# Kernel optimization log

Measured on AMD Instinct MI355X. Metric: run time of the kernel, lower is better.

## Reference

```python
import jax, jax.numpy as jnp
import numpy as np

FRAC_BITS = 16            # fixed-point fractional bits (MPC fixedpoint precision)
SCALE = float(1 << FRAC_BITS)

def fxp(v):
    """Emulate dup_with_precision: round value to the fixed-point grid with
    FRAC_BITS fractional bits. Straight-through (identity) gradient, matching
    the MPC backward pass which propagates gradients through truncation."""
    return v + jax.lax.stop_gradient(jnp.round(v * SCALE) / SCALE - v)


def setup_inputs() -> dict:
    key = jax.random.key(0)
    kx, kw = jax.random.split(key)
    in_dim, out_dim, batch = 4096, 4096, 2048
    x = jax.random.normal(kx, (batch, in_dim), dtype=jnp.float32)
    # Dense_Local init: w ~ N(0, 1/sqrt(in_dim+1)), b = zeros
    w = jax.random.normal(kw, (in_dim, out_dim), dtype=jnp.float32) / np.sqrt(in_dim + 1)
    b = jnp.zeros((out_dim,), dtype=jnp.float32)
    return {"x": x, "w": w, "b": b}


def reference(x, w, b):
    # quantize operands to the fixed-point grid (values live on the grid in MPC)
    xq = fxp(x)
    wq = fxp(w)
    # y = x @ w, then dup_with_precision(x.fixedpoint): truncate product back
    y = fxp(jnp.matmul(xq, wq))           # [batch, out_dim]
    # + bias
    y = y + fxp(b)
    # secure ReLU: s = drelu_local(y) (sign bit), y = relu(y, s) = y * s
    s = y >= 0
    y = jnp.where(s, y, jnp.zeros((), dtype=y.dtype))
    # final dup_with_precision(new_fixedpoint=x.fixedpoint)
    return fxp(y)
```

## Files before the change

### kernel.cpp

```cpp
#include <hip/hip_runtime.h>
#include <hip/hip_bf16.h>
#include <stdint.h>

#define M_DIM 2048
#define N_DIM 4096
#define K_DIM 4096

#define NT 64

typedef short short8 __attribute__((ext_vector_type(8)));
typedef float f32x4 __attribute__((ext_vector_type(4)));

typedef __attribute__((address_space(1))) unsigned int gu32;
typedef __attribute__((address_space(3))) unsigned int lu32;

__device__ static inline unsigned short f32_to_bf16(float f) {
  union { float f; unsigned int u; } v; v.f = f;
  unsigned int u = v.u;
  u += 0x7FFFu + ((u >> 16) & 1u);
  return (unsigned short)(u >> 16);
}

__global__ void cvt_x_kernel(const float* __restrict__ in, unsigned short* __restrict__ out) {
  size_t i = ((size_t)blockIdx.x * blockDim.x + threadIdx.x) * 8;
  f32x4 a = *(const f32x4*)(in + i);
  f32x4 b = *(const f32x4*)(in + i + 4);
  short8 o;
  o[0] = (short)f32_to_bf16(a[0]); o[1] = (short)f32_to_bf16(a[1]);
  o[2] = (short)f32_to_bf16(a[2]); o[3] = (short)f32_to_bf16(a[3]);
  o[4] = (short)f32_to_bf16(b[0]); o[5] = (short)f32_to_bf16(b[1]);
  o[6] = (short)f32_to_bf16(b[2]); o[7] = (short)f32_to_bf16(b[3]);
  *(short8*)(out + i) = o;
}

__global__ void transpose_cvt_w_kernel(const float* __restrict__ w, unsigned short* __restrict__ wt) {
  __shared__ unsigned short tile[64][64 + 8];
  int bn = blockIdx.x * 64;
  int bk = blockIdx.y * 64;
  int t = threadIdx.x;
  int c4 = (t & 15) * 4;
  int r0 = t >> 4;
#pragma unroll
  for (int p = 0; p < 4; ++p) {
    int r = r0 + p * 16;
    f32x4 v = *(const f32x4*)(w + (size_t)(bk + r) * N_DIM + bn + c4);
    tile[c4 + 0][r] = f32_to_bf16(v[0]);
    tile[c4 + 1][r] = f32_to_bf16(v[1]);
    tile[c4 + 2][r] = f32_to_bf16(v[2]);
    tile[c4 + 3][r] = f32_to_bf16(v[3]);
  }
  __syncthreads();
  int orow = t >> 2;
  int oc = (t & 3) * 16;
  short8 lo, hi;
#pragma unroll
  for (int j = 0; j < 8; ++j) {
    lo[j] = (short)tile[orow][oc + j];
    hi[j] = (short)tile[orow][oc + 8 + j];
  }
  unsigned short* op = wt + (size_t)(bn + orow) * K_DIM + bk + oc;
  *(short8*)(op) = lo;
  *(short8*)(op + 8) = hi;
}


__global__ __launch_bounds__(512) void gemm8_kernel(
    const unsigned short* __restrict__ A, const unsigned short* __restrict__ Bt,
    const float* __restrict__ bias, float* __restrict__ C) {
  __shared__ unsigned short smA[3 * 24576];
  char* smemc = (char*)&smA[0];

  const int tid = threadIdx.x;
  const int lane = tid & 63;
  const int w = tid >> 6;
  const int wm = w >> 2, wn = w & 3;

  const int id = blockIdx.x;
  const int x = id & 7, j = id >> 3;
  const int by = ((x >> 2) << 3) + (j >> 2);
  const int bx = ((x & 3) << 2) + (j & 3);
  const int r0 = by * 128, c0 = bx * 256;

  const int l8 = lane >> 3, l7 = lane & 7;
  const int chunkE = ((l7 ^ l8) << 3);
  const unsigned short* Ag = A + (size_t)(r0 + w * 16 + l8) * K_DIM + chunkE;
  const unsigned short* Bg = Bt + (size_t)(c0 + w * 32 + l8) * K_DIM + chunkE;
  const int aL0 = w * 2048;
  const int bL0 = 16384 + w * 4096;

#define GL(gp, ldsoff) __builtin_amdgcn_global_load_lds((gu32*)(gp), (lu32*)(smemc + (ldsoff)), 16, 0, 0)
#define STAGE_ALL(t, sb)                                               \
  do {                                                                 \
    GL(Ag + (size_t)(t) * 64, (sb) + aL0);                             \
    GL(Ag + (size_t)(t) * 64 + 8 * (size_t)K_DIM, (sb) + aL0 + 1024);  \
    GL(Bg + (size_t)(t) * 64, (sb) + bL0);                             \
    GL(Bg + (size_t)(t) * 64 + 8 * (size_t)K_DIM, (sb) + bL0 + 1024);  \
    GL(Bg + (size_t)(t) * 64 + 16 * (size_t)K_DIM, (sb) + bL0 + 2048); \
    GL(Bg + (size_t)(t) * 64 + 24 * (size_t)K_DIM, (sb) + bL0 + 3072); \
  } while (0)

  const int l15 = lane & 15, hi = lane >> 4;
  const int aR = (wm * 64 + l15) * 64;
  const int bR = 8192 + (wn * 64 + l15) * 64;
  const int slot0 = ((hi ^ l7) << 3);
  const int slot1 = (((4 + hi) ^ l7) << 3);
  const unsigned short* pA0s0 = smA + 0 * 24576 + aR + slot0;
  const unsigned short* pA1s0 = smA + 1 * 24576 + aR + slot0;
  const unsigned short* pA2s0 = smA + 2 * 24576 + aR + slot0;
  const unsigned short* pA0s1 = smA + 0 * 24576 + aR + slot1;
  const unsigned short* pA1s1 = smA + 1 * 24576 + aR + slot1;
  const unsigned short* pA2s1 = smA + 2 * 24576 + aR + slot1;
  const unsigned short* pB0s0 = smA + 0 * 24576 + bR + slot0;
  const unsigned short* pB1s0 = smA + 1 * 24576 + bR + slot0;
  const unsigned short* pB2s0 = smA + 2 * 24576 + bR + slot0;
  const unsigned short* pB0s1 = smA + 0 * 24576 + bR + slot1;
  const unsigned short* pB1s1 = smA + 1 * 24576 + bR + slot1;
  const unsigned short* pB2s1 = smA + 2 * 24576 + bR + slot1;

  f32x4 acc[4][4] = {};

  STAGE_ALL(0, 0);
  STAGE_ALL(1, 49152);

#define SGB __builtin_amdgcn_sched_group_barrier
  int cs = 0;
  for (int t = 0; t < NT; ++t) {
    const int stB = (cs == 0 ? 2 : cs - 1) * 49152;
    const bool doStage = (t + 2) < NT;

    const unsigned short* pAs0 = (cs == 0) ? pA0s0 : (cs == 1) ? pA1s0 : pA2s0;
    const unsigned short* pAs1 = (cs == 0) ? pA0s1 : (cs == 1) ? pA1s1 : pA2s1;
    const unsigned short* pBs0 = (cs == 0) ? pB0s0 : (cs == 1) ? pB1s0 : pB2s0;
    const unsigned short* pBs1 = (cs == 0) ? pB0s1 : (cs == 1) ? pB1s1 : pB2s1;

    if (t < NT - 1) asm volatile("s_waitcnt vmcnt(6) lgkmcnt(0)" ::: "memory");
    else            asm volatile("s_waitcnt vmcnt(0) lgkmcnt(0)" ::: "memory");
    asm volatile("s_barrier" ::: "memory");

    short8 a0[4], b0[4], a1[4], b1[4];
#pragma unroll
    for (int m = 0; m < 4; ++m) a0[m] = *(const short8*)(pAs0 + m * 1024);
#pragma unroll
    for (int n = 0; n < 4; ++n) b0[n] = *(const short8*)(pBs0 + n * 1024);
    if (doStage) STAGE_ALL(t + 2, stB);
#pragma unroll
    for (int m = 0; m < 4; ++m) a1[m] = *(const short8*)(pAs1 + m * 1024);
#pragma unroll
    for (int n = 0; n < 4; ++n) b1[n] = *(const short8*)(pBs1 + n * 1024);

    __builtin_amdgcn_s_setprio(1);
#pragma unroll
    for (int m = 0; m < 4; ++m)
#pragma unroll
      for (int n = 0; n < 4; ++n)
        acc[m][n] = __builtin_amdgcn_mfma_f32_16x16x32_bf16(a0[m], b0[n], acc[m][n], 0, 0, 0);
#pragma unroll
    for (int m = 0; m < 4; ++m)
#pragma unroll
      for (int n = 0; n < 4; ++n)
        acc[m][n] = __builtin_amdgcn_mfma_f32_16x16x32_bf16(a1[m], b1[n], acc[m][n], 0, 0, 0);
    __builtin_amdgcn_s_setprio(0);

    SGB(0x100, 8, 0);
    SGB(0x020, 6, 0);
    SGB(0x008, 2, 0); SGB(0x100, 1, 0);
    SGB(0x008, 2, 0); SGB(0x100, 1, 0);
    SGB(0x008, 2, 0); SGB(0x100, 1, 0);
    SGB(0x008, 2, 0); SGB(0x100, 1, 0);
    SGB(0x008, 2, 0); SGB(0x100, 1, 0);
    SGB(0x008, 2, 0); SGB(0x100, 1, 0);
    SGB(0x008, 2, 0); SGB(0x100, 1, 0);
    SGB(0x008, 2, 0); SGB(0x100, 1, 0);
    SGB(0x008, 16, 0);

    cs = (cs == 2) ? 0 : cs + 1;
  }
#undef SGB

  const float S = 65536.0f, IS = 1.0f / 65536.0f;
  const int lr = hi * 4;
#pragma unroll
  for (int n = 0; n < 4; ++n) {
    int gcol = c0 + wn * 64 + n * 16 + l15;
    float bq = rintf(bias[gcol] * S) * IS;
#pragma unroll
    for (int m = 0; m < 4; ++m) {
      int grow = r0 + wm * 64 + m * 16 + lr;
      float* outp = C + (size_t)grow * N_DIM + gcol;
#pragma unroll
      for (int r = 0; r < 4; ++r) {
        float t = rintf(acc[m][n][r] * S) * IS + bq;
        t = t > 0.0f ? t : 0.0f;
        outp[(size_t)r * N_DIM] = t;
      }
    }
  }
#undef GL
#undef STAGE_ALL
}

__global__ __launch_bounds__(256, 2) void gemm_fb_kernel(
    const float* __restrict__ Xf, const float* __restrict__ Wf,
    const float* __restrict__ bias, float* __restrict__ C) {
  __shared__ unsigned short As[128][64];
  __shared__ unsigned short Bs[128][64];
  int tid = threadIdx.x;
  int lane = tid & 63;
  int wid = tid >> 6;
  int wr = wid >> 1, wc = wid & 1;
  int r0 = blockIdx.y * 128;
  int c0 = blockIdx.x * 128;
  f32x4 acc[4][4] = {};
  for (int kt = 0; kt < K_DIM / 64; ++kt) {
    __syncthreads();
    int ar = tid >> 1;
    int ac = (tid & 1) * 32;
    const float* xp = Xf + (size_t)(r0 + ar) * K_DIM + kt * 64 + ac;
#pragma unroll
    for (int jj = 0; jj < 8; ++jj) {
      f32x4 v = *(const f32x4*)(xp + jj * 4);
      As[ar][ac + jj * 4 + 0] = f32_to_bf16(v[0]);
      As[ar][ac + jj * 4 + 1] = f32_to_bf16(v[1]);
      As[ar][ac + jj * 4 + 2] = f32_to_bf16(v[2]);
      As[ar][ac + jj * 4 + 3] = f32_to_bf16(v[3]);
    }
    int bk_ = tid >> 2;
    int bc = (tid & 3) * 32;
    const float* wp = Wf + (size_t)(kt * 64 + bk_) * N_DIM + c0 + bc;
#pragma unroll
    for (int jj = 0; jj < 8; ++jj) {
      f32x4 v = *(const f32x4*)(wp + jj * 4);
      Bs[bc + jj * 4 + 0][bk_] = f32_to_bf16(v[0]);
      Bs[bc + jj * 4 + 1][bk_] = f32_to_bf16(v[1]);
      Bs[bc + jj * 4 + 2][bk_] = f32_to_bf16(v[2]);
      Bs[bc + jj * 4 + 3][bk_] = f32_to_bf16(v[3]);
    }
    __syncthreads();
#pragma unroll
    for (int ks = 0; ks < 2; ++ks) {
      int co = ks * 32 + (lane >> 4) * 8;
      int rA = wr * 64 + (lane & 15);
      int rB = wc * 64 + (lane & 15);
      short8 a[4], b[4];
#pragma unroll
      for (int m = 0; m < 4; ++m) a[m] = *(const short8*)&As[rA + m * 16][co];
#pragma unroll
      for (int n = 0; n < 4; ++n) b[n] = *(const short8*)&Bs[rB + n * 16][co];
#pragma unroll
      for (int m = 0; m < 4; ++m)
#pragma unroll
        for (int n = 0; n < 4; ++n)
          acc[m][n] = __builtin_amdgcn_mfma_f32_16x16x32_bf16(a[m], b[n], acc[m][n], 0, 0, 0);
    }
  }
  const float S = 65536.0f, IS = 1.0f / 65536.0f;
  int lr = (lane >> 4) * 4;
  int lc = lane & 15;
#pragma unroll
  for (int n = 0; n < 4; ++n) {
    int gcol = c0 + wc * 64 + n * 16 + lc;
    float bq = rintf(bias[gcol] * S) * IS;
#pragma unroll
    for (int m = 0; m < 4; ++m) {
      int grow = r0 + wr * 64 + m * 16 + lr;
      float* outp = C + (size_t)grow * N_DIM + gcol;
#pragma unroll
      for (int r = 0; r < 4; ++r) {
        float t = rintf(acc[m][n][r] * S) * IS + bq;
        t = t > 0.0f ? t : 0.0f;
        outp[(size_t)r * N_DIM] = t;
      }
    }
  }
}

extern "C" void kernel_launch(void* const* d_in, const int* in_sizes, int n_in,
                              void* d_out, int out_size, void* d_ws, size_t ws_size,
                              hipStream_t stream) {
  const float* x = (const float*)d_in[0];
  const float* w = (const float*)d_in[1];
  const float* b = (const float*)d_in[2];
  float* out = (float*)d_out;

  size_t needA = (size_t)M_DIM * K_DIM * sizeof(unsigned short);
  size_t needB = (size_t)K_DIM * N_DIM * sizeof(unsigned short);

  if (ws_size >= needA + needB) {
    unsigned short* Abf = (unsigned short*)d_ws;
    unsigned short* Btbf = (unsigned short*)((char*)d_ws + needA);
    cvt_x_kernel<<<(M_DIM * (size_t)K_DIM / 8 + 255) / 256, 256, 0, stream>>>(x, Abf);
    transpose_cvt_w_kernel<<<dim3(N_DIM / 64, K_DIM / 64), 256, 0, stream>>>(w, Btbf);
    gemm8_kernel<<<256, 512, 0, stream>>>(Abf, Btbf, b, out);
  } else {
    gemm_fb_kernel<<<dim3(N_DIM / 128, M_DIM / 128), 256, 0, stream>>>(x, w, b, out);
  }
}
```

Measured before the change: 90.70 us.

## Split waves into two groups with staggered K-half order to overlap LDS reads and MFMA

Replaces the single load-all-then-compute body and its explicit sched_group_barrier interleaving with a two-phase body per K-half. Waves 0-3 process the first K half then the second, while waves 4-7 do the reverse, so the two groups issue LDS reads at different times and one group's reads can overlap the other's MFMAs. The fine-grained instruction scheduling hints are dropped and a sched_barrier is added before the workgroup barrier. The cost is branch divergence at wave granularity, and the compiler's schedule without hints may interleave loads and MFMAs less well.

```diff
diff --git a/kernel.cpp b/kernel.cpp
--- a/kernel.cpp
+++ b/kernel.cpp
@@ -122,7 +122,8 @@
   STAGE_ALL(0, 0);
   STAGE_ALL(1, 49152);
 
-#define SGB __builtin_amdgcn_sched_group_barrier
+  const bool grpB = (w >= 4);
+
   int cs = 0;
   for (int t = 0; t < NT; ++t) {
     const int stB = (cs == 0 ? 2 : cs - 1) * 49152;
@@ -135,47 +136,65 @@
 
     if (t < NT - 1) asm volatile("s_waitcnt vmcnt(6) lgkmcnt(0)" ::: "memory");
     else            asm volatile("s_waitcnt vmcnt(0) lgkmcnt(0)" ::: "memory");
+    __builtin_amdgcn_sched_barrier(0);
     asm volatile("s_barrier" ::: "memory");
 
-    short8 a0[4], b0[4], a1[4], b1[4];
-#pragma unroll
-    for (int m = 0; m < 4; ++m) a0[m] = *(const short8*)(pAs0 + m * 1024);
-#pragma unroll
-    for (int n = 0; n < 4; ++n) b0[n] = *(const short8*)(pBs0 + n * 1024);
-    if (doStage) STAGE_ALL(t + 2, stB);
-#pragma unroll
-    for (int m = 0; m < 4; ++m) a1[m] = *(const short8*)(pAs1 + m * 1024);
-#pragma unroll
-    for (int n = 0; n < 4; ++n) b1[n] = *(const short8*)(pBs1 + n * 1024);
-
-    __builtin_amdgcn_s_setprio(1);
-#pragma unroll
-    for (int m = 0; m < 4; ++m)
-#pragma unroll
-      for (int n = 0; n < 4; ++n)
-        acc[m][n] = __builtin_amdgcn_mfma_f32_16x16x32_bf16(a0[m], b0[n], acc[m][n], 0, 0, 0);
-#pragma unroll
-    for (int m = 0; m < 4; ++m)
-#pragma unroll
-      for (int n = 0; n < 4; ++n)
-        acc[m][n] = __builtin_amdgcn_mfma_f32_16x16x32_bf16(a1[m], b1[n], acc[m][n], 0, 0, 0);
-    __builtin_amdgcn_s_setprio(0);
-
-    SGB(0x100, 8, 0);
-    SGB(0x020, 6, 0);
-    SGB(0x008, 2, 0); SGB(0x100, 1, 0);
-    SGB(0x008, 2, 0); SGB(0x100, 1, 0);
-    SGB(0x008, 2, 0); SGB(0x100, 1, 0);
-    SGB(0x008, 2, 0); SGB(0x100, 1, 0);
-    SGB(0x008, 2, 0); SGB(0x100, 1, 0);
-    SGB(0x008, 2, 0); SGB(0x100, 1, 0);
-    SGB(0x008, 2, 0); SGB(0x100, 1, 0);
-    SGB(0x008, 2, 0); SGB(0x100, 1, 0);
-    SGB(0x008, 16, 0);
+    if (!grpB) {
+      short8 a0[4], b0[4];
+#pragma unroll
+      for (int m = 0; m < 4; ++m) a0[m] = *(const short8*)(pAs0 + m * 1024);
+#pragma unroll
+      for (int n = 0; n < 4; ++n) b0[n] = *(const short8*)(pBs0 + n * 1024);
+      if (doStage) STAGE_ALL(t + 2, stB);
+      __builtin_amdgcn_s_setprio(1);
+#pragma unroll
+      for (int m = 0; m < 4; ++m)
+#pragma unroll
+        for (int n = 0; n < 4; ++n)
+          acc[m][n] = __builtin_amdgcn_mfma_f32_16x16x32_bf16(a0[m], b0[n], acc[m][n], 0, 0, 0);
+      __builtin_amdgcn_s_setprio(0);
+      short8 a1[4], b1[4];
+#pragma unroll
+      for (int m = 0; m < 4; ++m) a1[m] = *(const short8*)(pAs1 + m * 1024);
+#pragma unroll
+      for (int n = 0; n < 4; ++n) b1[n] = *(const short8*)(pBs1 + n * 1024);
+      __builtin_amdgcn_s_setprio(1);
+#pragma unroll
+      for (int m = 0; m < 4; ++m)
+#pragma unroll
+        for (int n = 0; n < 4; ++n)
+          acc[m][n] = __builtin_amdgcn_mfma_f32_16x16x32_bf16(a1[m], b1[n], acc[m][n], 0, 0, 0);
+      __builtin_amdgcn_s_setprio(0);
+    } else {
+      short8 a1[4], b1[4];
+#pragma unroll
+      for (int m = 0; m < 4; ++m) a1[m] = *(const short8*)(pAs1 + m * 1024);
+#pragma unroll
+      for (int n = 0; n < 4; ++n) b1[n] = *(const short8*)(pBs1 + n * 1024);
+      if (doStage) STAGE_ALL(t + 2, stB);
+      __builtin_amdgcn_s_setprio(1);
+#pragma unroll
+      for (int m = 0; m < 4; ++m)
+#pragma unroll
+        for (int n = 0; n < 4; ++n)
+          acc[m][n] = __builtin_amdgcn_mfma_f32_16x16x32_bf16(a1[m], b1[n], acc[m][n], 0, 0, 0);
+      __builtin_amdgcn_s_setprio(0);
+      short8 a0[4], b0[4];
+#pragma unroll
+      for (int m = 0; m < 4; ++m) a0[m] = *(const short8*)(pAs0 + m * 1024);
+#pragma unroll
+      for (int n = 0; n < 4; ++n) b0[n] = *(const short8*)(pBs0 + n * 1024);
+      __builtin_amdgcn_s_setprio(1);
+#pragma unroll
+      for (int m = 0; m < 4; ++m)
+#pragma unroll
+        for (int n = 0; n < 4; ++n)
+          acc[m][n] = __builtin_amdgcn_mfma_f32_16x16x32_bf16(a0[m], b0[n], acc[m][n], 0, 0, 0);
+      __builtin_amdgcn_s_setprio(0);
+    }
 
     cs = (cs == 2) ? 0 : cs + 1;
   }
-#undef SGB
 
   const float S = 65536.0f, IS = 1.0f / 65536.0f;
   const int lr = hi * 4;
```

Result: no change. 92.21 us (+1.7%).
